# Performance work log

Measured on AMD Instinct MI355X. Metric: run time of the kernel, lower is better.

Reference implementation:

```python
import jax, jax.numpy as jnp
import numpy as np

B, C, H, W = 4, 64, 64, 64
RATIO = 8  # channel reduction in the channel-attention branch
C8 = C // RATIO


def conv1x1(x, Wt, b):
    # 1x1 conv == channel-mixing matmul. Wt: (out_c, in_c), x: (B, in_c, H, W)
    return jnp.einsum('oc,bchw->bohw', Wt, x) + b[None, :, None, None]


def setup_inputs() -> dict:
    key = jax.random.key(0)
    ks = jax.random.split(key, 12)
    s = 0.02
    return {
        'x': jax.random.normal(ks[0], (B, C, H, W), dtype=jnp.float32),
        'y': jax.random.normal(ks[1], (B, C, H, W), dtype=jnp.float32),
        'Wq': jax.random.normal(ks[2], (C, C), dtype=jnp.float32) * s,
        'bq': jnp.zeros((C,), dtype=jnp.float32),
        'Wk': jax.random.normal(ks[3], (C, C), dtype=jnp.float32) * s,
        'bk': jnp.zeros((C,), dtype=jnp.float32),
        'Wv': jax.random.normal(ks[4], (C, C), dtype=jnp.float32) * s,
        'bv': jnp.zeros((C,), dtype=jnp.float32),
        'Wq1': jax.random.normal(ks[5], (C8, C), dtype=jnp.float32) * s,
        'bq1': jnp.zeros((C8,), dtype=jnp.float32),
        'Wk1': jax.random.normal(ks[6], (C8, C), dtype=jnp.float32) * s,
        'bk1': jnp.zeros((C8,), dtype=jnp.float32),
    }


def reference(x, y, Wq, bq, Wk, bk, Wv, bv, Wq1, bq1, Wk1, bk1):
    b, c, h, w = x.shape
    hw = h * w
    # cross-attention branch: query from y, key/value from x
    Q = conv1x1(y, Wq, bq).reshape(b, c, hw)   # (B, C, HW)
    K = conv1x1(x, Wk, bk).reshape(b, c, hw)
    V = conv1x1(x, Wv, bv).reshape(b, c, hw)
    attn = jax.nn.softmax(jnp.einsum('bcq,bck->bqk', Q, K), axis=-1)  # (B, HW, HW)
    # channel-attention branch (PAM-style spatial map from x, ratio 8)
    Q1 = conv1x1(x, Wq1, bq1).reshape(b, C8, hw)
    K1 = conv1x1(x, Wk1, bk1).reshape(b, C8, hw)
    attn1 = jax.nn.softmax(jnp.einsum('bcq,bck->bqk', Q1, K1), axis=-1)  # (B, HW, HW)
    # out = attn @ V^T + attn1 @ V^T, shape (B, HW, C)
    out = jnp.einsum('bqk,bck->bqc', attn, V) + jnp.einsum('bqk,bck->bqc', attn1, V)
    return out.transpose(0, 2, 1).reshape(b, c, h, w)
```

## Files before the change

kernel.cpp:

```cpp
#include <hip/hip_runtime.h>
#include <hip/hip_bf16.h>


typedef __bf16 bf16x8 __attribute__((ext_vector_type(8)));
typedef float f32x16 __attribute__((ext_vector_type(16)));

#define MFMA32(A, B, C) __builtin_amdgcn_mfma_f32_32x32x16_bf16((A), (B), (C), 0, 0, 0)

#define LOG2E 1.4426950408889634f
#define EXP2F(x) __builtin_amdgcn_exp2f(x)

__device__ __forceinline__ uint4 ld16(const unsigned short* p) {
  return *reinterpret_cast<const uint4*>(p);
}
__device__ __forceinline__ bf16x8 asbf(uint4 v) {
  return __builtin_bit_cast(bf16x8, v);
}
__device__ __forceinline__ unsigned short f2bf(float f) {
  return __builtin_bit_cast(unsigned short, __float2bfloat16(f));
}
__device__ __forceinline__ unsigned pk2(float a, float b) {
  return (unsigned)f2bf(a) | ((unsigned)f2bf(b) << 16);
}

__global__ __launch_bounds__(256) void proj_kernel(
    const float* __restrict__ x, const float* __restrict__ y,
    const float* __restrict__ Wq, const float* __restrict__ bq,
    const float* __restrict__ Wk, const float* __restrict__ bk,
    const float* __restrict__ Wv, const float* __restrict__ bv,
    const float* __restrict__ Wq1, const float* __restrict__ bq1,
    const float* __restrict__ Wk1, const float* __restrict__ bk1,
    unsigned short* __restrict__ Qb, unsigned short* __restrict__ Kb,
    unsigned short* __restrict__ VtT, unsigned short* __restrict__ Q1c,
    unsigned short* __restrict__ K1c)
{
  __shared__ float ldsT[64][64];
  __shared__ float ldsW[64][65];
  __shared__ float ldsW2[64][65];
  __shared__ float ldsW1[8][64];
  __shared__ float ldsW1b[8][64];

  const int t = threadIdx.x;
  const int b = blockIdx.x >> 6;
  const int p0 = (blockIdx.x & 63) << 6;
  const int lane = t & 63;
  const int w = t >> 6;

  for (int i = t; i < 4096; i += 256) {
    int c = i >> 6, p = i & 63;
    ldsT[c][p] = y[(size_t)(b * 64 + c) * 4096 + p0 + p];
    ldsW[c][p] = Wq[i];
    ldsW2[c][p] = Wv[i];
  }
  for (int i = t; i < 512; i += 256) {
    ldsW1[i >> 6][i & 63] = Wq1[i];
    ldsW1b[i >> 6][i & 63] = Wk1[i];
  }
  __syncthreads();

  {
    float acc[16];
    float bias = bq[lane];
#pragma unroll
    for (int pp = 0; pp < 16; ++pp) acc[pp] = bias;
    for (int ic = 0; ic < 64; ++ic) {
      float wv_ = ldsW[lane][ic];
#pragma unroll
      for (int pp = 0; pp < 16; ++pp)
        acc[pp] = fmaf(wv_, ldsT[ic][w * 16 + pp], acc[pp]);
    }
#pragma unroll
    for (int pp = 0; pp < 16; ++pp)
      Qb[(size_t)(b * 4096 + p0 + w * 16 + pp) * 64 + lane] = f2bf(acc[pp] * LOG2E);
  }
  __syncthreads();

  for (int i = t; i < 4096; i += 256) {
    int c = i >> 6, p = i & 63;
    ldsT[c][p] = x[(size_t)(b * 64 + c) * 4096 + p0 + p];
    ldsW[c][p] = Wk[i];
  }
  __syncthreads();

  {
    float acc[16];
    float bias = bk[lane];
#pragma unroll
    for (int pp = 0; pp < 16; ++pp) acc[pp] = bias;
    for (int ic = 0; ic < 64; ++ic) {
      float wv_ = ldsW[lane][ic];
#pragma unroll
      for (int pp = 0; pp < 16; ++pp)
        acc[pp] = fmaf(wv_, ldsT[ic][w * 16 + pp], acc[pp]);
    }
#pragma unroll
    for (int pp = 0; pp < 16; ++pp)
      Kb[(size_t)(b * 4096 + p0 + w * 16 + pp) * 64 + lane] = f2bf(acc[pp]);
  }

  {
    float acc[16];
#pragma unroll
    for (int j = 0; j < 16; ++j) acc[j] = bv[16 * w + j];
    for (int ic = 0; ic < 64; ++ic) {
      float xv = ldsT[ic][lane];
#pragma unroll
      for (int j = 0; j < 16; ++j)
        acc[j] = fmaf(ldsW2[16 * w + j][ic], xv, acc[j]);
    }
    const int k = p0 + lane;
    const int kblk = k >> 5, ki = k & 31;
#pragma unroll
    for (int j = 0; j < 16; ++j)
      VtT[((size_t)(b * 128 + kblk) * 64 + 16 * w + j) * 32 + ki] = f2bf(acc[j]);
  }

  if (w == 0) {
    float acc[8];
#pragma unroll
    for (int j = 0; j < 8; ++j) acc[j] = bq1[j];
    for (int ic = 0; ic < 64; ++ic) {
      float xv = ldsT[ic][lane];
#pragma unroll
      for (int j = 0; j < 8; ++j)
        acc[j] = fmaf(ldsW1[j][ic], xv, acc[j]);
    }
    uint4 o;
    o.x = pk2(acc[0] * LOG2E, acc[1] * LOG2E);
    o.y = pk2(acc[2] * LOG2E, acc[3] * LOG2E);
    o.z = pk2(acc[4] * LOG2E, acc[5] * LOG2E);
    o.w = pk2(acc[6] * LOG2E, acc[7] * LOG2E);
    *reinterpret_cast<uint4*>(Q1c + (size_t)(b * 4096 + p0 + lane) * 8) = o;
  } else if (w == 1) {
    float acc[8];
#pragma unroll
    for (int j = 0; j < 8; ++j) acc[j] = bk1[j];
    for (int ic = 0; ic < 64; ++ic) {
      float xv = ldsT[ic][lane];
#pragma unroll
      for (int j = 0; j < 8; ++j)
        acc[j] = fmaf(ldsW1b[j][ic], xv, acc[j]);
    }
    uint4 o;
    o.x = pk2(acc[0], acc[1]); o.y = pk2(acc[2], acc[3]);
    o.z = pk2(acc[4], acc[5]); o.w = pk2(acc[6], acc[7]);
    *reinterpret_cast<uint4*>(K1c + (size_t)(b * 4096 + p0 + lane) * 8) = o;
  }
}

__global__ __launch_bounds__(512, 2) void attn_kernel(
    const unsigned short* __restrict__ Qb, const unsigned short* __restrict__ Kb,
    const unsigned short* __restrict__ VtT, const unsigned short* __restrict__ Q1c,
    const unsigned short* __restrict__ K1c, float* __restrict__ out)
{
  __shared__ float accbuf[2][2][64][32];
  __shared__ float zbuf[8][2][32];

  const int id = blockIdx.x;
  const int b = (id & 7) >> 1;
  const int qt = (id >> 3) + ((id & 1) << 6);
  const int q0 = qt * 32;

  const int wid = threadIdx.x >> 6;
  const int l = threadIdx.x & 63;
  const int qc = l & 31;
  const int h = l >> 5;

  const int kBeg = wid << 9;
  const int kEnd = kBeg + 512;

  const f32x16 zero16 = {0.f,0.f,0.f,0.f, 0.f,0.f,0.f,0.f,
                         0.f,0.f,0.f,0.f, 0.f,0.f,0.f,0.f};
  const uint4 zu4 = {0u, 0u, 0u, 0u};

  const unsigned short* qrow = Qb + (size_t)(b * 4096 + q0 + qc) * 64 + 8 * h;
  bf16x8 qf[4];
#pragma unroll
  for (int m = 0; m < 4; ++m) qf[m] = asbf(ld16(qrow + 16 * m));
  bf16x8 q1f;
  {
    uint4 v = zu4;
    if (h == 0) v = ld16(Q1c + (size_t)(b * 4096 + q0 + qc) * 8);
    q1f = asbf(v);
  }

  f32x16 accA0 = zero16, accA1 = zero16, accB0 = zero16, accB1 = zero16;
  float zA = 0.f, zB = 0.f;

#pragma unroll 1
  for (int k0 = kBeg; k0 < kEnd; k0 += 32) {
    uint4 kf[4], vf[4], k1f;
    {
      const unsigned short* kp = Kb + ((size_t)(b * 4096 + k0 + qc) << 6) + 8 * h;
      kf[0] = ld16(kp);
      kf[1] = ld16(kp + 16);
      kf[2] = ld16(kp + 32);
      kf[3] = ld16(kp + 48);
      k1f = zu4;
      if (h == 0) k1f = ld16(K1c + (size_t)(b * 4096 + k0 + qc) * 8);
      const unsigned short* vp =
          VtT + (((size_t)(b * 128 + (k0 >> 5)) * 64 + qc) << 5) + 8 * h;
      vf[0] = ld16(vp);
      vf[1] = ld16(vp + 16);
      vf[2] = ld16(vp + 32 * 32);
      vf[3] = ld16(vp + 32 * 32 + 16);
    }

    f32x16 sD = MFMA32(asbf(kf[0]), qf[0], zero16);
    sD = MFMA32(asbf(kf[1]), qf[1], sD);
    sD = MFMA32(asbf(kf[2]), qf[2], sD);
    sD = MFMA32(asbf(kf[3]), qf[3], sD);
    f32x16 uD = MFMA32(asbf(k1f), q1f, zero16);

#pragma unroll
    for (int r = 0; r < 16; ++r) { sD[r] = EXP2F(sD[r]); uD[r] = EXP2F(uD[r]); }
    zA += (((sD[0]+sD[1])+(sD[2]+sD[3])) + ((sD[4]+sD[5])+(sD[6]+sD[7]))) +
          (((sD[8]+sD[9])+(sD[10]+sD[11])) + ((sD[12]+sD[13])+(sD[14]+sD[15])));
    zB += (((uD[0]+uD[1])+(uD[2]+uD[3])) + ((uD[4]+uD[5])+(uD[6]+uD[7]))) +
          (((uD[8]+uD[9])+(uD[10]+uD[11])) + ((uD[12]+uD[13])+(uD[14]+uD[15])));

#pragma unroll
    for (int m = 0; m < 2; ++m) {
      unsigned W0 = pk2(sD[8*m+0], sD[8*m+1]);
      unsigned W1 = pk2(sD[8*m+2], sD[8*m+3]);
      unsigned W2 = pk2(sD[8*m+4], sD[8*m+5]);
      unsigned W3 = pk2(sD[8*m+6], sD[8*m+7]);
      auto s1 = __builtin_amdgcn_permlane32_swap((int)W0, (int)W2, false, false);
      auto s2 = __builtin_amdgcn_permlane32_swap((int)W1, (int)W3, false, false);
      uint4 pw;
      pw.x = (unsigned)s1[0]; pw.y = (unsigned)s2[0];
      pw.z = (unsigned)s1[1]; pw.w = (unsigned)s2[1];
      bf16x8 pf = asbf(pw);

      unsigned X0 = pk2(uD[8*m+0], uD[8*m+1]);
      unsigned X1 = pk2(uD[8*m+2], uD[8*m+3]);
      unsigned X2 = pk2(uD[8*m+4], uD[8*m+5]);
      unsigned X3 = pk2(uD[8*m+6], uD[8*m+7]);
      auto t1 = __builtin_amdgcn_permlane32_swap((int)X0, (int)X2, false, false);
      auto t2 = __builtin_amdgcn_permlane32_swap((int)X1, (int)X3, false, false);
      uint4 pw1;
      pw1.x = (unsigned)t1[0]; pw1.y = (unsigned)t2[0];
      pw1.z = (unsigned)t1[1]; pw1.w = (unsigned)t2[1];
      bf16x8 pf1 = asbf(pw1);

      accA0 = MFMA32(asbf(vf[m]),     pf,  accA0);
      accA1 = MFMA32(asbf(vf[2 + m]), pf,  accA1);
      accB0 = MFMA32(asbf(vf[m]),     pf1, accB0);
      accB1 = MFMA32(asbf(vf[2 + m]), pf1, accB1);
    }
  }

  zA += __shfl_xor(zA, 32);
  zB += __shfl_xor(zB, 32);
  if (h == 0) { zbuf[wid][0][qc] = zA; zbuf[wid][1][qc] = zB; }

  auto payload_write = [&](int slot) {
#pragma unroll
    for (int r = 0; r < 16; ++r) {
      const int c0 = (r & 3) + 8 * (r >> 2) + 4 * h;
      accbuf[slot][0][c0][qc]      = accA0[r];
      accbuf[slot][0][c0 + 32][qc] = accA1[r];
      accbuf[slot][1][c0][qc]      = accB0[r];
      accbuf[slot][1][c0 + 32][qc] = accB1[r];
    }
  };
  auto payload_add = [&](int slot) {
#pragma unroll
    for (int r = 0; r < 16; ++r) {
      const int c0 = (r & 3) + 8 * (r >> 2) + 4 * h;
      accA0[r] += accbuf[slot][0][c0][qc];
      accA1[r] += accbuf[slot][0][c0 + 32][qc];
      accB0[r] += accbuf[slot][1][c0][qc];
      accB1[r] += accbuf[slot][1][c0 + 32][qc];
    }
  };

  if (wid == 1) payload_write(0);
  if (wid == 5) payload_write(1);
  __syncthreads();
  if (wid == 0) payload_add(0);
  if (wid == 4) payload_add(1);
  __syncthreads();
  if (wid == 3) payload_write(0);
  if (wid == 7) payload_write(1);
  __syncthreads();
  if (wid == 2) payload_add(0);
  if (wid == 6) payload_add(1);
  __syncthreads();
  if (wid == 2) payload_write(0);
  if (wid == 6) payload_write(1);
  __syncthreads();
  if (wid == 0) payload_add(0);
  if (wid == 4) payload_add(1);
  __syncthreads();
  if (wid == 4) payload_write(0);
  __syncthreads();
  if (wid == 0) {
    payload_add(0);
    float zAt = 0.f, zBt = 0.f;
#pragma unroll
    for (int ww = 0; ww < 8; ++ww) { zAt += zbuf[ww][0][qc]; zBt += zbuf[ww][1][qc]; }
    const float rA = 1.0f / zAt, rB = 1.0f / zBt;
    float* op = out + (size_t)b * (64 * 4096) + q0 + qc;
#pragma unroll
    for (int r = 0; r < 16; ++r) {
      const int c0 = (r & 3) + 8 * (r >> 2) + 4 * h;
      op[(size_t)c0 * 4096]        = accA0[r] * rA + accB0[r] * rB;
      op[(size_t)(c0 + 32) * 4096] = accA1[r] * rA + accB1[r] * rB;
    }
  }
}

extern "C" void kernel_launch(void* const* d_in, const int* in_sizes, int n_in,
                              void* d_out, int out_size, void* d_ws, size_t ws_size,
                              hipStream_t stream) {
  (void)in_sizes; (void)n_in; (void)out_size; (void)ws_size;
  const float* x = (const float*)d_in[0];
  const float* y = (const float*)d_in[1];
  const float* Wq = (const float*)d_in[2];
  const float* bq = (const float*)d_in[3];
  const float* Wk = (const float*)d_in[4];
  const float* bk = (const float*)d_in[5];
  const float* Wv = (const float*)d_in[6];
  const float* bv = (const float*)d_in[7];
  const float* Wq1 = (const float*)d_in[8];
  const float* bq1 = (const float*)d_in[9];
  const float* Wk1 = (const float*)d_in[10];
  const float* bk1 = (const float*)d_in[11];

  char* ws = (char*)d_ws;
  unsigned short* Qb = (unsigned short*)(ws);
  unsigned short* Kb = (unsigned short*)(ws + (2u << 20));
  unsigned short* VtT = (unsigned short*)(ws + (4u << 20));
  unsigned short* Q1c = (unsigned short*)(ws + (6u << 20));
  unsigned short* K1c = (unsigned short*)(ws + (6u << 20) + (256u << 10));

  proj_kernel<<<256, 256, 0, stream>>>(x, y, Wq, bq, Wk, bk, Wv, bv,
                                       Wq1, bq1, Wk1, bk1, Qb, Kb, VtT, Q1c, K1c);
  attn_kernel<<<512, 512, 0, stream>>>(Qb, Kb, VtT, Q1c, K1c, (float*)d_out);
}
```

Measured before the change: 82.73 us.

## Halve projection tile, use packed bf16 convert asm, and raise MFMA priority

```diff
diff --git a/kernel.cpp b/kernel.cpp
--- a/kernel.cpp
+++ b/kernel.cpp
@@ -19,8 +19,10 @@
 __device__ __forceinline__ unsigned short f2bf(float f) {
   return __builtin_bit_cast(unsigned short, __float2bfloat16(f));
 }
-__device__ __forceinline__ unsigned pk2(float a, float b) {
-  return (unsigned)f2bf(a) | ((unsigned)f2bf(b) << 16);
+__device__ __forceinline__ unsigned cvtpk(float a, float b) {
+  unsigned r;
+  asm("v_cvt_pk_bf16_f32 %0, %1, %2" : "=v"(r) : "v"(a), "v"(b));
+  return r;
 }
 
 __global__ __launch_bounds__(256) void proj_kernel(
@@ -34,21 +36,24 @@
     unsigned short* __restrict__ VtT, unsigned short* __restrict__ Q1c,
     unsigned short* __restrict__ K1c)
 {
-  __shared__ float ldsT[64][64];
+  __shared__ float ldsT[64][32];
   __shared__ float ldsW[64][65];
   __shared__ float ldsW2[64][65];
   __shared__ float ldsW1[8][64];
   __shared__ float ldsW1b[8][64];
 
   const int t = threadIdx.x;
-  const int b = blockIdx.x >> 6;
-  const int p0 = (blockIdx.x & 63) << 6;
+  const int b = blockIdx.x >> 7;
+  const int p0 = (blockIdx.x & 127) << 5;
   const int lane = t & 63;
   const int w = t >> 6;
 
+  for (int i = t; i < 2048; i += 256) {
+    int c = i >> 5, p = i & 31;
+    ldsT[c][p] = y[(size_t)(b * 64 + c) * 4096 + p0 + p];
+  }
   for (int i = t; i < 4096; i += 256) {
     int c = i >> 6, p = i & 63;
-    ldsT[c][p] = y[(size_t)(b * 64 + c) * 4096 + p0 + p];
     ldsW[c][p] = Wq[i];
     ldsW2[c][p] = Wv[i];
   }
@@ -59,63 +64,69 @@
   __syncthreads();
 
   {
-    float acc[16];
+    float acc[8];
     float bias = bq[lane];
 #pragma unroll
-    for (int pp = 0; pp < 16; ++pp) acc[pp] = bias;
+    for (int pp = 0; pp < 8; ++pp) acc[pp] = bias;
     for (int ic = 0; ic < 64; ++ic) {
       float wv_ = ldsW[lane][ic];
 #pragma unroll
-      for (int pp = 0; pp < 16; ++pp)
-        acc[pp] = fmaf(wv_, ldsT[ic][w * 16 + pp], acc[pp]);
-    }
-#pragma unroll
-    for (int pp = 0; pp < 16; ++pp)
-      Qb[(size_t)(b * 4096 + p0 + w * 16 + pp) * 64 + lane] = f2bf(acc[pp] * LOG2E);
-  }
-  __syncthreads();
-
+      for (int pp = 0; pp < 8; ++pp)
+        acc[pp] = fmaf(wv_, ldsT[ic][w * 8 + pp], acc[pp]);
+    }
+#pragma unroll
+    for (int pp = 0; pp < 8; ++pp)
+      Qb[(size_t)(b * 4096 + p0 + w * 8 + pp) * 64 + lane] = f2bf(acc[pp] * LOG2E);
+  }
+  __syncthreads();
+
+  for (int i = t; i < 2048; i += 256) {
+    int c = i >> 5, p = i & 31;
+    ldsT[c][p] = x[(size_t)(b * 64 + c) * 4096 + p0 + p];
+  }
   for (int i = t; i < 4096; i += 256) {
     int c = i >> 6, p = i & 63;
-    ldsT[c][p] = x[(size_t)(b * 64 + c) * 4096 + p0 + p];
     ldsW[c][p] = Wk[i];
   }
   __syncthreads();
 
   {
-    float acc[16];
+    float acc[8];
     float bias = bk[lane];
 #pragma unroll
-    for (int pp = 0; pp < 16; ++pp) acc[pp] = bias;
+    for (int pp = 0; pp < 8; ++pp) acc[pp] = bias;
     for (int ic = 0; ic < 64; ++ic) {
       float wv_ = ldsW[lane][ic];
 #pragma unroll
-      for (int pp = 0; pp < 16; ++pp)
-        acc[pp] = fmaf(wv_, ldsT[ic][w * 16 + pp], acc[pp]);
-    }
-#pragma unroll
-    for (int pp = 0; pp < 16; ++pp)
-      Kb[(size_t)(b * 4096 + p0 + w * 16 + pp) * 64 + lane] = f2bf(acc[pp]);
+      for (int pp = 0; pp < 8; ++pp)
+        acc[pp] = fmaf(wv_, ldsT[ic][w * 8 + pp], acc[pp]);
+    }
+#pragma unroll
+    for (int pp = 0; pp < 8; ++pp)
+      Kb[(size_t)(b * 4096 + p0 + w * 8 + pp) * 64 + lane] = f2bf(acc[pp]);
   }
 
   {
-    float acc[16];
-#pragma unroll
-    for (int j = 0; j < 16; ++j) acc[j] = bv[16 * w + j];
-    for (int ic = 0; ic < 64; ++ic) {
-      float xv = ldsT[ic][lane];
-#pragma unroll
-      for (int j = 0; j < 16; ++j)
-        acc[j] = fmaf(ldsW2[16 * w + j][ic], xv, acc[j]);
-    }
-    const int k = p0 + lane;
+    const int half = lane >> 5;
+    const int px = lane & 31;
+    const int oc0 = 16 * w + 8 * half;
+    float acc[8];
+#pragma unroll
+    for (int j = 0; j < 8; ++j) acc[j] = bv[oc0 + j];
+    for (int ic = 0; ic < 64; ++ic) {
+      float xv = ldsT[ic][px];
+#pragma unroll
+      for (int j = 0; j < 8; ++j)
+        acc[j] = fmaf(ldsW2[oc0 + j][ic], xv, acc[j]);
+    }
+    const int k = p0 + px;
     const int kblk = k >> 5, ki = k & 31;
 #pragma unroll
-    for (int j = 0; j < 16; ++j)
-      VtT[((size_t)(b * 128 + kblk) * 64 + 16 * w + j) * 32 + ki] = f2bf(acc[j]);
-  }
-
-  if (w == 0) {
+    for (int j = 0; j < 8; ++j)
+      VtT[((size_t)(b * 128 + kblk) * 64 + oc0 + j) * 32 + ki] = f2bf(acc[j]);
+  }
+
+  if (w == 0 && lane < 32) {
     float acc[8];
 #pragma unroll
     for (int j = 0; j < 8; ++j) acc[j] = bq1[j];
@@ -126,12 +137,12 @@
         acc[j] = fmaf(ldsW1[j][ic], xv, acc[j]);
     }
     uint4 o;
-    o.x = pk2(acc[0] * LOG2E, acc[1] * LOG2E);
-    o.y = pk2(acc[2] * LOG2E, acc[3] * LOG2E);
-    o.z = pk2(acc[4] * LOG2E, acc[5] * LOG2E);
-    o.w = pk2(acc[6] * LOG2E, acc[7] * LOG2E);
+    o.x = cvtpk(acc[0] * LOG2E, acc[1] * LOG2E);
+    o.y = cvtpk(acc[2] * LOG2E, acc[3] * LOG2E);
+    o.z = cvtpk(acc[4] * LOG2E, acc[5] * LOG2E);
+    o.w = cvtpk(acc[6] * LOG2E, acc[7] * LOG2E);
     *reinterpret_cast<uint4*>(Q1c + (size_t)(b * 4096 + p0 + lane) * 8) = o;
-  } else if (w == 1) {
+  } else if (w == 1 && lane < 32) {
     float acc[8];
 #pragma unroll
     for (int j = 0; j < 8; ++j) acc[j] = bk1[j];
@@ -142,8 +153,8 @@
         acc[j] = fmaf(ldsW1b[j][ic], xv, acc[j]);
     }
     uint4 o;
-    o.x = pk2(acc[0], acc[1]); o.y = pk2(acc[2], acc[3]);
-    o.z = pk2(acc[4], acc[5]); o.w = pk2(acc[6], acc[7]);
+    o.x = cvtpk(acc[0], acc[1]); o.y = cvtpk(acc[2], acc[3]);
+    o.z = cvtpk(acc[4], acc[5]); o.w = cvtpk(acc[6], acc[7]);
     *reinterpret_cast<uint4*>(K1c + (size_t)(b * 4096 + p0 + lane) * 8) = o;
   }
 }
@@ -206,11 +217,13 @@
       vf[3] = ld16(vp + 32 * 32 + 16);
     }
 
+    __builtin_amdgcn_s_setprio(1);
     f32x16 sD = MFMA32(asbf(kf[0]), qf[0], zero16);
     sD = MFMA32(asbf(kf[1]), qf[1], sD);
     sD = MFMA32(asbf(kf[2]), qf[2], sD);
     sD = MFMA32(asbf(kf[3]), qf[3], sD);
     f32x16 uD = MFMA32(asbf(k1f), q1f, zero16);
+    __builtin_amdgcn_s_setprio(0);
 
 #pragma unroll
     for (int r = 0; r < 16; ++r) { sD[r] = EXP2F(sD[r]); uD[r] = EXP2F(uD[r]); }
@@ -221,10 +234,10 @@
 
 #pragma unroll
     for (int m = 0; m < 2; ++m) {
-      unsigned W0 = pk2(sD[8*m+0], sD[8*m+1]);
-      unsigned W1 = pk2(sD[8*m+2], sD[8*m+3]);
-      unsigned W2 = pk2(sD[8*m+4], sD[8*m+5]);
-      unsigned W3 = pk2(sD[8*m+6], sD[8*m+7]);
+      unsigned W0 = cvtpk(sD[8*m+0], sD[8*m+1]);
+      unsigned W1 = cvtpk(sD[8*m+2], sD[8*m+3]);
+      unsigned W2 = cvtpk(sD[8*m+4], sD[8*m+5]);
+      unsigned W3 = cvtpk(sD[8*m+6], sD[8*m+7]);
       auto s1 = __builtin_amdgcn_permlane32_swap((int)W0, (int)W2, false, false);
       auto s2 = __builtin_amdgcn_permlane32_swap((int)W1, (int)W3, false, false);
       uint4 pw;
@@ -232,10 +245,10 @@
       pw.z = (unsigned)s1[1]; pw.w = (unsigned)s2[1];
       bf16x8 pf = asbf(pw);
 
-      unsigned X0 = pk2(uD[8*m+0], uD[8*m+1]);
-      unsigned X1 = pk2(uD[8*m+2], uD[8*m+3]);
-      unsigned X2 = pk2(uD[8*m+4], uD[8*m+5]);
-      unsigned X3 = pk2(uD[8*m+6], uD[8*m+7]);
+      unsigned X0 = cvtpk(uD[8*m+0], uD[8*m+1]);
+      unsigned X1 = cvtpk(uD[8*m+2], uD[8*m+3]);
+      unsigned X2 = cvtpk(uD[8*m+4], uD[8*m+5]);
+      unsigned X3 = cvtpk(uD[8*m+6], uD[8*m+7]);
       auto t1 = __builtin_amdgcn_permlane32_swap((int)X0, (int)X2, false, false);
       auto t2 = __builtin_amdgcn_permlane32_swap((int)X1, (int)X3, false, false);
       uint4 pw1;
@@ -243,10 +256,12 @@
       pw1.z = (unsigned)t1[1]; pw1.w = (unsigned)t2[1];
       bf16x8 pf1 = asbf(pw1);
 
+      __builtin_amdgcn_s_setprio(1);
       accA0 = MFMA32(asbf(vf[m]),     pf,  accA0);
       accA1 = MFMA32(asbf(vf[2 + m]), pf,  accA1);
       accB0 = MFMA32(asbf(vf[m]),     pf1, accB0);
       accB1 = MFMA32(asbf(vf[2 + m]), pf1, accB1);
+      __builtin_amdgcn_s_setprio(0);
     }
   }
 
@@ -335,7 +350,7 @@
   unsigned short* Q1c = (unsigned short*)(ws + (6u << 20));
   unsigned short* K1c = (unsigned short*)(ws + (6u << 20) + (256u << 10));
 
-  proj_kernel<<<256, 256, 0, stream>>>(x, y, Wq, bq, Wk, bk, Wv, bv,
+  proj_kernel<<<512, 256, 0, stream>>>(x, y, Wq, bq, Wk, bk, Wv, bv,
                                        Wq1, bq1, Wk1, bk1, Qb, Kb, VtT, Q1c, K1c);
   attn_kernel<<<512, 512, 0, stream>>>(Qb, Kb, VtT, Q1c, K1c, (float*)d_out);
 }
```

Result: faster. 79.48 us (-3.9%).
